# Performance work log

Hardware: AMD Instinct MI355X
Metric: run time of the kernel (lower is better)

## Reference

```python
import jax, jax.numpy as jnp
import numpy as np

B, IN_CH, OUT_CH, N_GRID, MODES = 64, 64, 64, 2048, 512


def _dct1_matrix(N, dtype=jnp.float32):
    """Matrix M s.t. (x @ M.T) == scipy.fftpack.dct(x, type=1, axis=-1).
    DCT-I: y[k] = x[0] + (-1)^k x[N-1] + 2*sum_{n=1}^{N-2} x[n] cos(pi k n/(N-1)).
    Note scipy's unnormalized idct(type=1) is the same transform, so M also
    implements chebyshev_inverse."""
    k = jnp.arange(N, dtype=jnp.float32)
    M = jnp.cos(jnp.pi * jnp.outer(k, k) / (N - 1))
    c = jnp.full((N,), 2.0, dtype=jnp.float32).at[0].set(1.0).at[N - 1].set(1.0)
    return (M * c[None, :]).astype(dtype)


def setup_inputs() -> dict:
    key = jax.random.key(0)
    kx, kw = jax.random.split(key)
    x = jax.random.normal(kx, (B, IN_CH, N_GRID), dtype=jnp.float32)
    # xavier_uniform on (in, out, modes): fan_in=in, fan_out=out (per torch for 3D params)
    bound = float(np.sqrt(6.0 / (IN_CH + OUT_CH)))
    weights = jax.random.uniform(kw, (IN_CH, OUT_CH, MODES), minval=-bound,
                                 maxval=bound, dtype=jnp.float32)
    return {"x": x, "weights": weights}


def reference(x, weights):
    # x: [b, in, n]; weights: [in, out, modes]
    N = x.shape[-1]
    modes = weights.shape[-1]
    M = _dct1_matrix(N, x.dtype)
    # forward Chebyshev (DCT-I) transform along grid axis
    x_cheb = jnp.einsum('bin,kn->bik', x, M)          # [b, in, n]
    # mix modes: keep first `modes` coefficients, zero the rest
    out_modes = jnp.einsum('bix,iox->box', x_cheb[..., :modes], weights)
    out_cheb = jnp.pad(out_modes, ((0, 0), (0, 0), (0, N - modes)))
    # inverse transform (scipy unnormalized IDCT-I == DCT-I)
    return jnp.einsum('bok,nk->bon', out_cheb, M)     # [b, out, n]
```

## Files before the change

### kernel.cpp

```cpp
#include <hip/hip_runtime.h>

typedef unsigned short u16;
typedef __attribute__((ext_vector_type(8))) short short8;
typedef __attribute__((ext_vector_type(4))) float f32x4;

#define B_  64
#define IC  64
#define OC  64
#define NG  2048
#define MD  512

__device__ inline u16 f2b(float f) {
  unsigned u = __float_as_uint(f);
  unsigned r = (u + 0x7FFFu + ((u >> 16) & 1u)) >> 16;
  return (u16)r;
}

__device__ __forceinline__ float cosk(int k, int n) {
  int r = (k * n) % (2 * (NG - 1));
  return __cosf((float)r * (3.14159265358979323846f / (NG - 1)));
}

__device__ __forceinline__ void gld_lds16(const u16* g, const u16* l) {
  __builtin_amdgcn_global_load_lds(
      (__attribute__((address_space(1))) void*)(uintptr_t)(g),
      (__attribute__((address_space(3))) void*)(unsigned)(uintptr_t)(l),
      16, 0, 0);
}

__global__ __launch_bounds__(256) void prep(
    const float* __restrict__ x, const float* __restrict__ w,
    u16* __restrict__ e, u16* __restrict__ o, u16* __restrict__ wT2,
    u16* __restrict__ M1p, u16* __restrict__ M3e, u16* __restrict__ M3o) {
  __shared__ float S[64][65];
  const int id = blockIdx.x;
  const int t = threadIdx.x;
  if (id < 4096) {
    const float* xr = x + (size_t)id * NG;
    float4 f = *(const float4*)(xr + 4 * t);
    float4 b = *(const float4*)(xr + (2044 - 4 * t));
    ushort4 ev, ov;
    ev.x = f2b(f.x + b.w); ov.x = f2b(f.x - b.w);
    ev.y = f2b(f.y + b.z); ov.y = f2b(f.y - b.z);
    ev.z = f2b(f.z + b.y); ov.z = f2b(f.z - b.y);
    ev.w = f2b(f.w + b.x); ov.w = f2b(f.w - b.x);
    *(ushort4*)(e + (size_t)id * 1024 + 4 * t) = ev;
    *(ushort4*)(o + (size_t)id * 1024 + 4 * t) = ov;
  } else if (id < 4608) {
    int wb = id - 4096;
    int oo = wb & 63, kb = wb >> 6;
    int r0 = t >> 6, c = t & 63;
#pragma unroll
    for (int j = 0; j < 16; ++j) {
      int i = r0 + j * 4;
      S[i][c] = w[(size_t)(i * 64 + oo) * MD + kb * 64 + c];
    }
    __syncthreads();
#pragma unroll
    for (int j = 0; j < 16; ++j) {
      int kk = r0 + j * 4;
      wT2[(size_t)(kb * 64 + kk) * 4096 + oo * 64 + c] = f2b(S[c][kk]);
    }
  } else if (id < 6656) {
    int idx = (id - 4608) * 256 + t;
    int r = idx >> 10, n = idx & 1023;
    int k = (r < 256) ? 2 * r : 2 * (r - 256) + 1;
    float v = cosk(k, n) * ((n == 0) ? 1.0f : 2.0f);
    M1p[idx] = f2b(v);
  } else {
    int idx = (id - 6656) * 256 + t;
    int half = idx >> 18;
    int rem = idx & 262143;
    int n = rem >> 8, kp = rem & 255;
    if (half == 0) {
      float v = cosk(2 * kp, n) * ((kp == 0) ? 1.0f : 2.0f);
      M3e[rem] = f2b(v);
    } else {
      float v = cosk(2 * kp + 1, n) * 2.0f;
      M3o[rem] = f2b(v);
    }
  }
}

template<int MI, int NI, bool OUT_BF16>
__global__ __launch_bounds__(256, 2) void gemm_bt3(
    const u16* __restrict__ A,
    const u16* __restrict__ Bt0,
    const u16* __restrict__ Bt1,
    int splitY,
    void* __restrict__ Cv,
    int K, int N) {
  constexpr int TM = MI * 32;
  constexpr int TN = NI * 32;
  constexpr int BK = 64;
  constexpr int ROWS = TM + TN;
  constexpr int CH = ROWS / 4;
  constexpr int NISSUE = CH / 8;
  constexpr int BUF = ROWS * BK;
  __shared__ u16 S[2 * BUF];

  const int tid  = threadIdx.x;
  const int lane = tid & 63;
  const int wave = tid >> 6;
  const int wm = (wave >> 1) * (MI * 16);
  const int wn = (wave & 1) * (NI * 16);
  const long bm = (long)blockIdx.y * TM;
  const long bn = (long)blockIdx.x * TN;
  const u16* Bt = ((int)blockIdx.y < splitY) ? Bt0 : Bt1;

  const int lrow = lane & 15;
  const int lhi  = lane >> 4;

  const int scc = (((lane & 7) ^ (lane >> 3)) * 8);
  const int r0 = wave * CH;

  const u16* gsrc[NISSUE];
  unsigned lofs[NISSUE];
#pragma unroll
  for (int ii = 0; ii < NISSUE; ++ii) {
    int rr = r0 + ii * 8 + (lane >> 3);
    gsrc[ii] = (rr < TM) ? (A + (bm + rr) * (long)K + scc)
                         : (Bt + (bn + rr - TM) * (long)K + scc);
    lofs[ii] = (unsigned)((r0 + ii * 8) * BK);
  }

  f32x4 acc[MI][NI] = {};

#pragma unroll
  for (int ii = 0; ii < NISSUE; ++ii)
    gld_lds16(gsrc[ii], &S[lofs[ii]]);

  int p = 0;
  for (int k0 = 0; k0 < K; k0 += BK) {
    __syncthreads();

    if (k0 + BK < K) {
#pragma unroll
      for (int ii = 0; ii < NISSUE; ++ii)
        gld_lds16(gsrc[ii] + k0 + BK, &S[(1 - p) * BUF + lofs[ii]]);
    }

    const u16* Sp = &S[p * BUF];
#pragma unroll
    for (int kk8 = 0; kk8 < 8; kk8 += 4) {
      short8 af[MI], bfr[NI];
#pragma unroll
      for (int i = 0; i < MI; ++i) {
        int pch = ((kk8 + lhi) ^ (lane & 7));
        af[i] = *(const short8*)&Sp[(wm + i * 16 + lrow) * BK + pch * 8];
      }
#pragma unroll
      for (int j = 0; j < NI; ++j) {
        int pch = ((kk8 + lhi) ^ (lane & 7));
        bfr[j] = *(const short8*)&Sp[(TM + wn + j * 16 + lrow) * BK + pch * 8];
      }
#pragma unroll
      for (int i = 0; i < MI; ++i)
#pragma unroll
        for (int j = 0; j < NI; ++j)
          acc[i][j] = __builtin_amdgcn_mfma_f32_16x16x32_bf16(af[i], bfr[j], acc[i][j], 0, 0, 0);
    }
    p ^= 1;
  }

  const int crow = (lane >> 4) * 4;
  const int ccol = lane & 15;
#pragma unroll
  for (int i = 0; i < MI; ++i)
#pragma unroll
    for (int j = 0; j < NI; ++j) {
      long gm = bm + wm + i * 16 + crow;
      long gn = bn + wn + j * 16 + ccol;
      if (OUT_BF16) {
        u16* cp = (u16*)Cv + gm * (long)N + gn;
#pragma unroll
        for (int r = 0; r < 4; ++r)
          cp[(long)r * N] = f2b(acc[i][j][r]);
      } else {
        float* cp = (float*)Cv + gm * (long)N + gn;
#pragma unroll
        for (int r = 0; r < 4; ++r)
          cp[(long)r * N] = acc[i][j][r];
      }
    }
}

__global__ __launch_bounds__(256, 4) void mode_mix_mfma(
    const u16* __restrict__ xcT,
    const u16* __restrict__ wT2,
    u16* __restrict__ omT) {
  constexpr int PK = 72;
  __shared__ u16 S[128 * PK];
  const int k = blockIdx.x;
  const int rk = (k & 1) ? 256 + (k >> 1) : (k >> 1);
  const int t = threadIdx.x;

#pragma unroll
  for (int c = 0; c < 4; ++c) {
    int ch = t + c * 256;
    int half = ch >> 9, cc = ch & 511;
    int row = cc >> 3, col8 = cc & 7;
    const u16* src = half ? (wT2 + (size_t)k * 4096)
                          : (xcT + (size_t)rk * 4096);
    uint4 v = *(const uint4*)(src + row * 64 + col8 * 8);
    *(uint4*)&S[(half * 64 + row) * PK + col8 * 8] = v;
  }
  __syncthreads();

  const int lane = t & 63;
  const int wave = t >> 6;
  const int wm = (wave >> 1) * 32;
  const int wn = (wave & 1) * 32;
  const int lrow = lane & 15;
  const int lhi  = lane >> 4;

  f32x4 acc[2][2] = {};
#pragma unroll
  for (int kk8 = 0; kk8 < 8; kk8 += 4) {
    short8 af[2], bfr[2];
#pragma unroll
    for (int i = 0; i < 2; ++i)
      af[i] = *(const short8*)&S[(wm + i * 16 + lrow) * PK + (kk8 + lhi) * 8];
#pragma unroll
    for (int j = 0; j < 2; ++j)
      bfr[j] = *(const short8*)&S[(64 + wn + j * 16 + lrow) * PK + (kk8 + lhi) * 8];
#pragma unroll
    for (int i = 0; i < 2; ++i)
#pragma unroll
      for (int j = 0; j < 2; ++j)
        acc[i][j] = __builtin_amdgcn_mfma_f32_16x16x32_bf16(af[i], bfr[j], acc[i][j], 0, 0, 0);
  }

  const int crow = (lane >> 4) * 4;
  const int ccol = lane & 15;
#pragma unroll
  for (int i = 0; i < 2; ++i)
#pragma unroll
    for (int j = 0; j < 2; ++j) {
      int b = wm + i * 16 + crow;
      int oo = wn + j * 16 + ccol;
#pragma unroll
      for (int r = 0; r < 4; ++r)
        omT[(size_t)k * 4096 + (b + r) * 64 + oo] = f2b(acc[i][j][r]);
    }
}

__global__ __launch_bounds__(256) void transpose_om(const u16* __restrict__ omT,
                                                    u16* __restrict__ omp) {
  __shared__ u16 S[64][65];
  const int bb = blockIdx.x;
  const int kb = blockIdx.y;
  const int t = threadIdx.x;
  const int r0 = t >> 6;
  const int c  = t & 63;
#pragma unroll
  for (int j = 0; j < 16; ++j) {
    int kr = r0 + j * 4;
    S[kr][c] = omT[(size_t)(kb * 64 + kr) * 4096 + bb * 64 + c];
  }
  __syncthreads();
  const int col = ((c & 1) ? 256 : 0) + kb * 32 + (c >> 1);
#pragma unroll
  for (int j = 0; j < 16; ++j) {
    int br = r0 + j * 4;
    omp[(size_t)(bb * 64 + br) * MD + col] = S[c][br];
  }
}

__global__ __launch_bounds__(256, 2) void gemm_g3(
    const u16* __restrict__ omp,
    const u16* __restrict__ M3e,
    const u16* __restrict__ M3o,
    float* __restrict__ out) {
  constexpr int BK = 64;
  constexpr int ROWS = 384;
  constexpr int CH = ROWS / 4;
  constexpr int NISSUE = CH / 8;
  __shared__ u16 S[ROWS * BK];

  const int tid  = threadIdx.x;
  const int lane = tid & 63;
  const int wave = tid >> 6;
  const long bm = (long)blockIdx.y * 128;
  const int n0 = blockIdx.x * 64;

  const int lrow = lane & 15;
  const int lhi  = lane >> 4;
  const int scc = (((lane & 7) ^ (lane >> 3)) * 8);
  const int r0 = wave * CH;

  const u16* gsrc[NISSUE];
  unsigned lofs[NISSUE];
#pragma unroll
  for (int ii = 0; ii < NISSUE; ++ii) {
    int rr = r0 + ii * 8 + (lane >> 3);
    const u16* p;
    if (rr < 128)       p = omp + (bm + rr) * (long)512 + scc;
    else if (rr < 256)  p = omp + (bm + rr - 128) * (long)512 + 256 + scc;
    else if (rr < 320)  p = M3e + (n0 + rr - 256) * (long)256 + scc;
    else                p = M3o + (n0 + rr - 320) * (long)256 + scc;
    gsrc[ii] = p;
    lofs[ii] = (unsigned)((r0 + ii * 8) * BK);
  }

  f32x4 accE[2][4] = {};
  f32x4 accO[2][4] = {};

  for (int k0 = 0; k0 < 256; k0 += BK) {
#pragma unroll
    for (int ii = 0; ii < NISSUE; ++ii)
      gld_lds16(gsrc[ii] + k0, &S[lofs[ii]]);
    __syncthreads();

#pragma unroll
    for (int kk8 = 0; kk8 < 8; kk8 += 4) {
      int pch = ((kk8 + lhi) ^ (lane & 7));
      short8 aE[2], aO[2], bE[4], bO[4];
#pragma unroll
      for (int i = 0; i < 2; ++i) {
        aE[i] = *(const short8*)&S[(wave * 32 + i * 16 + lrow) * BK + pch * 8];
        aO[i] = *(const short8*)&S[(128 + wave * 32 + i * 16 + lrow) * BK + pch * 8];
      }
#pragma unroll
      for (int j = 0; j < 4; ++j) {
        bE[j] = *(const short8*)&S[(256 + j * 16 + lrow) * BK + pch * 8];
        bO[j] = *(const short8*)&S[(320 + j * 16 + lrow) * BK + pch * 8];
      }
#pragma unroll
      for (int i = 0; i < 2; ++i)
#pragma unroll
        for (int j = 0; j < 4; ++j) {
          accE[i][j] = __builtin_amdgcn_mfma_f32_16x16x32_bf16(aE[i], bE[j], accE[i][j], 0, 0, 0);
          accO[i][j] = __builtin_amdgcn_mfma_f32_16x16x32_bf16(aO[i], bO[j], accO[i][j], 0, 0, 0);
        }
    }
    __syncthreads();
  }

  const int crow = (lane >> 4) * 4;
  const int ccol = lane & 15;
#pragma unroll
  for (int i = 0; i < 2; ++i)
#pragma unroll
    for (int j = 0; j < 4; ++j) {
      long bo = bm + wave * 32 + i * 16 + crow;
      int n = n0 + j * 16 + ccol;
      float* op = out + bo * (long)NG;
#pragma unroll
      for (int r = 0; r < 4; ++r) {
        float E = accE[i][j][r], O = accO[i][j][r];
        op[(long)r * NG + n] = E + O;
        op[(long)r * NG + (NG - 1 - n)] = E - O;
      }
    }
}

extern "C" void kernel_launch(void* const* d_in, const int* in_sizes, int n_in,
                              void* d_out, int out_size, void* d_ws, size_t ws_size,
                              hipStream_t stream) {
  const float* x = (const float*)d_in[0];
  const float* w = (const float*)d_in[1];
  float* out = (float*)d_out;

  char* ws = (char*)d_ws;
  u16* e    = (u16*)ws;
  u16* o    = (u16*)(ws + (size_t)8 * 1024 * 1024);
  u16* M1p  = (u16*)(ws + (size_t)16 * 1024 * 1024);
  u16* M3e  = (u16*)(ws + (size_t)17 * 1024 * 1024);
  u16* M3o  = (u16*)(ws + (size_t)17 * 1024 * 1024 + 512 * 1024);
  u16* xcT  = (u16*)(ws + (size_t)20 * 1024 * 1024);
  u16* wT2  = (u16*)(ws + (size_t)24 * 1024 * 1024);
  u16* omT  = (u16*)(ws + (size_t)28 * 1024 * 1024);
  u16* omp  = (u16*)(ws + (size_t)32 * 1024 * 1024);

  prep<<<8704, 256, 0, stream>>>(x, w, e, o, wT2, M1p, M3e, M3o);

  gemm_bt3<2, 2, true><<<dim3((B_ * IC) / 64, 512 / 64), 256, 0, stream>>>(
      M1p, e, o, 4, xcT, 1024, B_ * IC);

  mode_mix_mfma<<<MD, 256, 0, stream>>>(xcT, wT2, omT);

  transpose_om<<<dim3((B_ * OC) / 64, MD / 64), 256, 0, stream>>>(omT, omp);

  gemm_g3<<<dim3(1024 / 64, (B_ * OC) / 128), 256, 0, stream>>>(omp, M3e, M3o, out);
}
```

Measured before the change: 118.0 us.

## Replace forward DCT GEMM with single-wave 64x64 tile kernel

The forward Chebyshev GEMM now runs one 64-thread wave per 64x64 output tile, using a 4x4 MFMA register tile per wave instead of four waves each holding 2x2. Each wave reuses more A/B fragments from LDS per load and needs no inter-wave coordination, at the cost of higher register pressure. Blocks are also much smaller, so fewer waves per CU are available to hide global-to-LDS latency. Dimensions are hardcoded as constants.

```diff
diff --git a/kernel.cpp b/kernel.cpp
--- a/kernel.cpp
+++ b/kernel.cpp
@@ -82,106 +82,81 @@
   }
 }
 
-template<int MI, int NI, bool OUT_BF16>
-__global__ __launch_bounds__(256, 2) void gemm_bt3(
+__global__ __launch_bounds__(64) void gemm_g1(
     const u16* __restrict__ A,
     const u16* __restrict__ Bt0,
     const u16* __restrict__ Bt1,
-    int splitY,
-    void* __restrict__ Cv,
-    int K, int N) {
-  constexpr int TM = MI * 32;
-  constexpr int TN = NI * 32;
+    u16* __restrict__ C) {
+  constexpr int K = 1024;
   constexpr int BK = 64;
-  constexpr int ROWS = TM + TN;
-  constexpr int CH = ROWS / 4;
-  constexpr int NISSUE = CH / 8;
-  constexpr int BUF = ROWS * BK;
+  constexpr int BUF = 128 * BK;
   __shared__ u16 S[2 * BUF];
 
-  const int tid  = threadIdx.x;
-  const int lane = tid & 63;
-  const int wave = tid >> 6;
-  const int wm = (wave >> 1) * (MI * 16);
-  const int wn = (wave & 1) * (NI * 16);
-  const long bm = (long)blockIdx.y * TM;
-  const long bn = (long)blockIdx.x * TN;
-  const u16* Bt = ((int)blockIdx.y < splitY) ? Bt0 : Bt1;
+  const int lane = threadIdx.x;
+  const long bm = (long)blockIdx.y * 64;
+  const long bn = (long)blockIdx.x * 64;
+  const u16* Bt = ((int)blockIdx.y < 4) ? Bt0 : Bt1;
 
   const int lrow = lane & 15;
   const int lhi  = lane >> 4;
-
   const int scc = (((lane & 7) ^ (lane >> 3)) * 8);
-  const int r0 = wave * CH;
-
-  const u16* gsrc[NISSUE];
-  unsigned lofs[NISSUE];
-#pragma unroll
-  for (int ii = 0; ii < NISSUE; ++ii) {
-    int rr = r0 + ii * 8 + (lane >> 3);
-    gsrc[ii] = (rr < TM) ? (A + (bm + rr) * (long)K + scc)
-                         : (Bt + (bn + rr - TM) * (long)K + scc);
-    lofs[ii] = (unsigned)((r0 + ii * 8) * BK);
-  }
-
-  f32x4 acc[MI][NI] = {};
-
-#pragma unroll
-  for (int ii = 0; ii < NISSUE; ++ii)
-    gld_lds16(gsrc[ii], &S[lofs[ii]]);
+
+  const u16* Ab = A  + (bm + (lane >> 3)) * (long)K + scc;
+  const u16* Bb = Bt + (bn + (lane >> 3)) * (long)K + scc;
+
+  f32x4 acc[4][4] = {};
+
+#pragma unroll
+  for (int ii = 0; ii < 8; ++ii) {
+    gld_lds16(Ab + (long)ii * 8 * K, &S[ii * 8 * BK]);
+    gld_lds16(Bb + (long)ii * 8 * K, &S[(64 + ii * 8) * BK]);
+  }
 
   int p = 0;
   for (int k0 = 0; k0 < K; k0 += BK) {
     __syncthreads();
 
     if (k0 + BK < K) {
-#pragma unroll
-      for (int ii = 0; ii < NISSUE; ++ii)
-        gld_lds16(gsrc[ii] + k0 + BK, &S[(1 - p) * BUF + lofs[ii]]);
+      const unsigned bo = (unsigned)((1 - p) * BUF);
+#pragma unroll
+      for (int ii = 0; ii < 8; ++ii) {
+        gld_lds16(Ab + (long)ii * 8 * K + k0 + BK, &S[bo + ii * 8 * BK]);
+        gld_lds16(Bb + (long)ii * 8 * K + k0 + BK, &S[bo + (64 + ii * 8) * BK]);
+      }
     }
 
     const u16* Sp = &S[p * BUF];
 #pragma unroll
     for (int kk8 = 0; kk8 < 8; kk8 += 4) {
-      short8 af[MI], bfr[NI];
-#pragma unroll
-      for (int i = 0; i < MI; ++i) {
-        int pch = ((kk8 + lhi) ^ (lane & 7));
-        af[i] = *(const short8*)&Sp[(wm + i * 16 + lrow) * BK + pch * 8];
-      }
-#pragma unroll
-      for (int j = 0; j < NI; ++j) {
-        int pch = ((kk8 + lhi) ^ (lane & 7));
-        bfr[j] = *(const short8*)&Sp[(TM + wn + j * 16 + lrow) * BK + pch * 8];
-      }
-#pragma unroll
-      for (int i = 0; i < MI; ++i)
-#pragma unroll
-        for (int j = 0; j < NI; ++j)
+      const int pchA = (kk8 + lhi) ^ (lrow & 7);
+      short8 af[4], bfr[4];
+#pragma unroll
+      for (int i = 0; i < 4; ++i)
+        af[i] = *(const short8*)&Sp[(i * 16 + lrow) * BK + pchA * 8];
+#pragma unroll
+      for (int j = 0; j < 4; ++j)
+        bfr[j] = *(const short8*)&Sp[(64 + j * 16 + lrow) * BK + pchA * 8];
+#pragma unroll
+      for (int i = 0; i < 4; ++i)
+#pragma unroll
+        for (int j = 0; j < 4; ++j)
           acc[i][j] = __builtin_amdgcn_mfma_f32_16x16x32_bf16(af[i], bfr[j], acc[i][j], 0, 0, 0);
     }
     p ^= 1;
   }
 
-  const int crow = (lane >> 4) * 4;
+  const int crow = lhi * 4;
   const int ccol = lane & 15;
 #pragma unroll
-  for (int i = 0; i < MI; ++i)
-#pragma unroll
-    for (int j = 0; j < NI; ++j) {
-      long gm = bm + wm + i * 16 + crow;
-      long gn = bn + wn + j * 16 + ccol;
-      if (OUT_BF16) {
-        u16* cp = (u16*)Cv + gm * (long)N + gn;
-#pragma unroll
-        for (int r = 0; r < 4; ++r)
-          cp[(long)r * N] = f2b(acc[i][j][r]);
-      } else {
-        float* cp = (float*)Cv + gm * (long)N + gn;
-#pragma unroll
-        for (int r = 0; r < 4; ++r)
-          cp[(long)r * N] = acc[i][j][r];
-      }
+  for (int i = 0; i < 4; ++i)
+#pragma unroll
+    for (int j = 0; j < 4; ++j) {
+      long gm = bm + i * 16 + crow;
+      long gn = bn + j * 16 + ccol;
+      u16* cp = C + gm * (long)4096 + gn;
+#pragma unroll
+      for (int r = 0; r < 4; ++r)
+        cp[(long)r * 4096] = f2b(acc[i][j][r]);
     }
 }
 
@@ -375,8 +350,7 @@
 
   prep<<<8704, 256, 0, stream>>>(x, w, e, o, wT2, M1p, M3e, M3o);
 
-  gemm_bt3<2, 2, true><<<dim3((B_ * IC) / 64, 512 / 64), 256, 0, stream>>>(
-      M1p, e, o, 4, xcT, 1024, B_ * IC);
+  gemm_g1<<<dim3((B_ * IC) / 64, 512 / 64), 64, 0, stream>>>(M1p, e, o, xcT);
 
   mode_mix_mfma<<<MD, 256, 0, stream>>>(xcT, wT2, omT);
 
```

Measured after the change: 119.1 us. Within noise of the previous version (+1.0%).
